# Performance work log

Measured on AMD Instinct MI355X. Metric: run time of the kernel, lower is better.

Reference implementation:

```python
import jax, jax.numpy as jnp
import numpy as np

NEG_SLOPE = 0.2
EPS = 1e-16


def sp_gat_layer(h, src, trg, w, a_src, a_trg):
    # h: [N, f_in], w: [H, f_in, f_out], a_src/a_trg: [H, f_out]
    n = h.shape[0]
    h_prime = jnp.einsum('nf,hfo->nho', h, w)            # [N, H, O]
    attn_src = jnp.einsum('nho,ho->nh', h_prime, a_src)  # [N, H]
    attn_trg = jnp.einsum('nho,ho->nh', h_prime, a_trg)  # [N, H]
    e = jax.nn.leaky_relu(attn_src[src] + attn_trg[trg], NEG_SLOPE)  # [E, H]
    e = e - e.max()  # global max-shift, as in the torch code
    exp_e = jnp.exp(e)
    denom = jax.ops.segment_sum(exp_e, trg, num_segments=n)          # [N, H]
    neigh_attn = exp_e / (denom[trg] + EPS)                          # [E, H]
    h_weighted = h_prime[src] * neigh_attn[..., None]                # [E, H, O]
    return jax.ops.segment_sum(h_weighted, trg, num_segments=n)     # [N, H, O]


def run_stack(h, src, trg, params):
    # params: list of (w, a_src, a_trg); last layer mean over heads, others elu+flatten
    n = h.shape[0]
    n_layers = len(params)
    for i, (w, a_src, a_trg) in enumerate(params):
        out = sp_gat_layer(h, src, trg, w, a_src, a_trg)  # [N, H, O]
        if i + 1 == n_layers:
            h = out.mean(axis=1)                          # [N, O]
        else:
            h = jax.nn.elu(out.reshape(n, -1))            # [N, H*O]
    return h


def setup_inputs() -> dict:
    key = jax.random.key(0)
    ks = jax.random.split(key, 24)
    N, E = 60000, 800000
    H, F0, O = 8, 128, 32
    inp = {
        'h0': jax.random.normal(ks[0], (N, F0), jnp.float32),
        'h1': jax.random.normal(ks[1], (N, F0), jnp.float32),
        'src0': jax.random.randint(ks[2], (E,), 0, N),
        'trg0': jax.random.randint(ks[3], (E,), 0, N),
        'src1': jax.random.randint(ks[4], (E,), 0, N),
        'trg1': jax.random.randint(ks[5], (E,), 0, N),
        'w00': jax.random.normal(ks[6], (H, F0, O), jnp.float32) * 0.1,
        'asrc00': jax.random.normal(ks[7], (H, O), jnp.float32) * 0.1,
        'atrg00': jax.random.normal(ks[8], (H, O), jnp.float32) * 0.1,
        'w01': jax.random.normal(ks[9], (H, H * O, O), jnp.float32) * 0.1,
        'asrc01': jax.random.normal(ks[10], (H, O), jnp.float32) * 0.1,
        'atrg01': jax.random.normal(ks[11], (H, O), jnp.float32) * 0.1,
        'w10': jax.random.normal(ks[12], (H, F0, O), jnp.float32) * 0.1,
        'asrc10': jax.random.normal(ks[13], (H, O), jnp.float32) * 0.1,
        'atrg10': jax.random.normal(ks[14], (H, O), jnp.float32) * 0.1,
        'w11': jax.random.normal(ks[15], (H, H * O, O), jnp.float32) * 0.1,
        'asrc11': jax.random.normal(ks[16], (H, O), jnp.float32) * 0.1,
        'atrg11': jax.random.normal(ks[17], (H, O), jnp.float32) * 0.1,
        'fc_w': jax.random.normal(ks[18], (2 * O, 2), jnp.float32) * 0.1,
        'fc_b': jnp.zeros((2,), jnp.float32),
    }
    return inp


N_USER = 50000


def reference(h0, h1, src0, trg0, src1, trg1,
              w00, asrc00, atrg00, w01, asrc01, atrg01,
              w10, asrc10, atrg10, w11, asrc11, atrg11,
              fc_w, fc_b):
    emb0 = run_stack(h0, src0, trg0, [(w00, asrc00, atrg00), (w01, asrc01, atrg01)])
    emb1 = run_stack(h1, src1, trg1, [(w10, asrc10, atrg10), (w11, asrc11, atrg11)])
    ret = jnp.concatenate([emb0[:N_USER], emb1[:N_USER]], axis=-1)  # [n_user, 64]
    logits = ret @ fc_w + fc_b
    return jax.nn.log_softmax(logits, axis=-1)
```

## Files before the change

### kernel.cpp

```cpp
#include <hip/hip_runtime.h>
#include <math.h>

#define H 8
#define O 32
#define C 256
#define CAP 48
#define NEG_SLOPE 0.2f
#define EPS_V 1e-16f
#define LOG2E 1.4426950408889634f

#define W_BKT 128
#define NB_PAD 512
#define BCAP 2048
#define EPB 4096

typedef float f32x4 __attribute__((ext_vector_type(4)));
typedef float f32x2 __attribute__((ext_vector_type(2)));
typedef short bf16x8 __attribute__((ext_vector_type(8)));

__device__ __forceinline__ unsigned short f2bf(float x){
  unsigned u = __float_as_uint(x);
  unsigned r = (u + 0x7fffu + ((u >> 16) & 1u)) >> 16;
  return (unsigned short)r;
}
__device__ __forceinline__ float bf2f(unsigned short u){
  return __uint_as_float((unsigned)u << 16);
}

template<int F>
__device__ __forceinline__ void cvt_a_body(const float* __restrict__ src,
                                           short* __restrict__ dst,
                                           int n_nodes, int t, int total){
  constexpr int KB = F / 8;
  if (t >= total) return;
  int kb = t % KB;
  int m  = (t / KB) & 15;
  int rt = t / (KB * 16);
  int row = rt * 16 + m;
  float v[8];
  if (row < n_nodes){
    const float4 p0 = *(const float4*)(src + (size_t)row * F + kb * 8);
    const float4 p1 = *(const float4*)(src + (size_t)row * F + kb * 8 + 4);
    v[0]=p0.x; v[1]=p0.y; v[2]=p0.z; v[3]=p0.w;
    v[4]=p1.x; v[5]=p1.y; v[6]=p1.z; v[7]=p1.w;
  } else {
    for (int j = 0; j < 8; ++j) v[j] = 0.f;
  }
  bf16x8 o;
  for (int j = 0; j < 8; ++j) o[j] = (short)f2bf(v[j]);
  *(bf16x8*)(dst + (((size_t)rt * KB + kb) * 16 + m) * 8) = o;
}

template<int F>
__device__ __forceinline__ void cvt_w_body(const float* __restrict__ w,
                                           short* __restrict__ wb, int t){
  constexpr int KB = F / 8;
  if (t >= 256 * KB) return;
  int c = t & 255, kb = t >> 8;
  int h = c >> 5, o = c & 31;
  bf16x8 out;
  for (int j = 0; j < 8; ++j){
    int f = kb * 8 + j;
    out[j] = (short)f2bf(w[((size_t)h * F + f) * O + o]);
  }
  *(bf16x8*)(wb + ((size_t)kb * 256 + c) * 8) = out;
}

__device__ void pass1_body(const int* __restrict__ trg, const int* __restrict__ src,
                           unsigned* __restrict__ gbuf, unsigned* __restrict__ gcur,
                           int E, int bx, int tid){
  __shared__ int cnt[NB_PAD];
  __shared__ int offl[NB_PAD];
  __shared__ unsigned baseg[NB_PAD];
  __shared__ int cur[NB_PAD];
  __shared__ unsigned payload[EPB];

  const int e0 = bx * EPB;
  const int ne = min(EPB, E - e0);
  for (int i = tid; i < NB_PAD; i += 256) cnt[i] = 0;
  __syncthreads();
  for (int i = tid; i < ne; i += 256){
    int t = trg[e0 + i];
    atomicAdd(&cnt[t >> 7], 1);
  }
  __syncthreads();
  for (int i = tid; i < NB_PAD; i += 256){
    int c = cnt[i];
    baseg[i] = c ? atomicAdd(&gcur[i], (unsigned)c) : 0u;
  }
  if (tid < 64){
    int v[8]; int s = 0;
#pragma unroll
    for (int j = 0; j < 8; ++j){ v[j] = cnt[tid * 8 + j]; s += v[j]; }
    int x = s;
#pragma unroll
    for (int d = 1; d < 64; d <<= 1){
      int o = __shfl_up(x, d, 64);
      if (tid >= d) x += o;
    }
    int base = x - s;
#pragma unroll
    for (int j = 0; j < 8; ++j){ offl[tid * 8 + j] = base; base += v[j]; }
  }
  __syncthreads();
  for (int i = tid; i < NB_PAD; i += 256) cur[i] = offl[i];
  __syncthreads();
  for (int i = tid; i < ne; i += 256){
    int t = trg[e0 + i];
    int s = src[e0 + i];
    int b = t >> 7;
    int p = atomicAdd(&cur[b], 1);
    payload[p] = ((unsigned)b << 23) | ((unsigned)(t & 127) << 16) | (unsigned)s;
  }
  __syncthreads();
  for (int i = tid; i < ne; i += 256){
    unsigned v = payload[i];
    unsigned b = v >> 23;
    unsigned pos = baseg[b] + (unsigned)(i - offl[b]);
    if (pos < BCAP) gbuf[(size_t)b * BCAP + pos] = v;
  }
}

__device__ void pass2_body(const unsigned* __restrict__ gbuf,
                           const unsigned* __restrict__ gcur,
                           unsigned short* __restrict__ csrc, int* __restrict__ degv,
                           int N, int bx, int tid){
  __shared__ unsigned short ell[W_BKT * CAP];
  __shared__ int dcnt[W_BKT];
  const int node0 = bx << 7;
  const int nn = min(W_BKT, N - node0);
  const unsigned pat = ((unsigned)N << 16) | (unsigned)N;
  unsigned* e32 = (unsigned*)ell;
  for (int i = tid; i < W_BKT * CAP / 2; i += 256) e32[i] = pat;
  for (int i = tid; i < W_BKT; i += 256) dcnt[i] = 0;
  __syncthreads();
  const int ne = min((int)gcur[bx], BCAP);
  for (int i = tid; i < ne; i += 256){
    unsigned v = gbuf[(size_t)bx * BCAP + i];
    int lt = (v >> 16) & 127;
    int p = atomicAdd(&dcnt[lt], 1);
    if (p < CAP) ell[lt * CAP + p] = (unsigned short)(v & 0xffffu);
  }
  __syncthreads();
  const uint4* s4 = (const uint4*)ell;
  uint4* d4 = (uint4*)(csrc + (size_t)node0 * CAP);
  const int n16 = nn * (CAP / 8);
  for (int i = tid; i < n16; i += 256) d4[i] = s4[i];
  for (int i = tid; i < nn; i += 256) degv[node0 + i] = dcnt[i];
}

template<int F>
__device__ __forceinline__ void gemm_body(
    const short* __restrict__ hb, const short* __restrict__ wb,
    const float* __restrict__ a_src, const float* __restrict__ a_trg,
    unsigned char* __restrict__ hp, float* __restrict__ as_, float* __restrict__ at_,
    int n_nodes, int bx, int tidx){
  constexpr int KB = F / 8;
  const int w = tidx >> 6, l = tidx & 63;
  const int q = l >> 4, m15 = l & 15;
  const int row0 = bx * 32;
  const size_t rt0 = row0 >> 4;
  const int ct0 = w * 4;
  float wsv[4], wtv[4];
#pragma unroll
  for (int ct = 0; ct < 4; ++ct){
    int col = (ct0 + ct) * 16 + m15;
    wsv[ct] = a_src[col];
    wtv[ct] = a_trg[col];
  }
  f32x4 acc[2][4] = {};
  for (int kk = 0; kk < F / 32; ++kk){
    const int kb0 = kk * 4 + q;
    bf16x8 a0 = *(const bf16x8*)(hb + ((rt0 * KB + kb0) * 16 + m15) * 8);
    bf16x8 a1 = *(const bf16x8*)(hb + (((rt0 + 1) * KB + kb0) * 16 + m15) * 8);
    const short* wp = wb + ((size_t)kb0 * 256 + ct0 * 16 + m15) * 8;
#pragma unroll
    for (int ct = 0; ct < 4; ++ct){
      bf16x8 b = *(const bf16x8*)(wp + ct * 128);
      acc[0][ct] = __builtin_amdgcn_mfma_f32_16x16x32_bf16(a0, b, acc[0][ct], 0, 0, 0);
      acc[1][ct] = __builtin_amdgcn_mfma_f32_16x16x32_bf16(a1, b, acc[1][ct], 0, 0, 0);
    }
  }
  float att[2][4][4] = {};
#pragma unroll
  for (int rt2 = 0; rt2 < 2; ++rt2){
    int nb = row0 + rt2 * 16 + q * 4;
#pragma unroll
    for (int ct = 0; ct < 4; ++ct){
      int col = (ct0 + ct) * 16 + m15;
      int hi = ct >> 1;
      int p01 = __builtin_amdgcn_cvt_pk_fp8_f32(acc[rt2][ct][0], acc[rt2][ct][1], 0, false);
      int p23 = __builtin_amdgcn_cvt_pk_fp8_f32(acc[rt2][ct][2], acc[rt2][ct][3], 0, false);
      unsigned char qb[4] = {(unsigned char)(p01 & 0xff),
                             (unsigned char)((p01 >> 8) & 0xff),
                             (unsigned char)(p23 & 0xff),
                             (unsigned char)((p23 >> 8) & 0xff)};
#pragma unroll
      for (int r = 0; r < 4; ++r){
        int n = nb + r;
        if (n < n_nodes) hp[(size_t)n * C + col] = qb[r];
        float vr = acc[rt2][ct][r];
        att[rt2][r][hi]     = fmaf(vr, wsv[ct], att[rt2][r][hi]);
        att[rt2][r][2 + hi] = fmaf(vr, wtv[ct], att[rt2][r][2 + hi]);
      }
    }
  }
#pragma unroll
  for (int rt2 = 0; rt2 < 2; ++rt2)
#pragma unroll
    for (int r = 0; r < 4; ++r)
#pragma unroll
      for (int k = 0; k < 4; ++k){
        float v = att[rt2][r][k];
        v += __shfl_xor(v, 1, 64);
        v += __shfl_xor(v, 2, 64);
        v += __shfl_xor(v, 4, 64);
        v += __shfl_xor(v, 8, 64);
        att[rt2][r][k] = v;
      }
  if (m15 == 0){
    int h0i = 2 * w;
#pragma unroll
    for (int rt2 = 0; rt2 < 2; ++rt2){
      int nb = row0 + rt2 * 16 + q * 4;
#pragma unroll
      for (int r = 0; r < 4; ++r){
        int n = nb + r;
        if (n < n_nodes){
          as_[n * H + h0i]     = att[rt2][r][0] * LOG2E;
          as_[n * H + h0i + 1] = att[rt2][r][1] * LOG2E;
          at_[n * H + h0i]     = att[rt2][r][2] * LOG2E;
          at_[n * H + h0i + 1] = att[rt2][r][3] * LOG2E;
        }
      }
    }
  }
}

__global__ void prep_kernel(
    const float* __restrict__ h0, const float* __restrict__ h1,
    const float* __restrict__ w000, const float* __restrict__ w100,
    const float* __restrict__ w001, const float* __restrict__ w101,
    const int* __restrict__ t0, const int* __restrict__ t1,
    const int* __restrict__ s0, const int* __restrict__ s1,
    short* __restrict__ hb, short* __restrict__ wb0, short* __restrict__ wb1,
    unsigned* __restrict__ gbuf, unsigned* __restrict__ gcur,
    float* __restrict__ as_,
    int N, int E, int tot_a, int cvtaB, int p1B,
    size_t hbStride, size_t wbStride, size_t asStride){
  int y = blockIdx.y;
  int bx = blockIdx.x;
  int tid = threadIdx.x;
  if (bx < cvtaB){
    cvt_a_body<128>(y ? h1 : h0, hb + (size_t)y * hbStride, N, bx * 256 + tid, tot_a);
    return;
  }
  bx -= cvtaB;
  if (bx < 16){
    cvt_w_body<128>(y ? w100 : w000, wb0 + (size_t)y * wbStride, bx * 256 + tid);
    return;
  }
  bx -= 16;
  if (bx < 32){
    cvt_w_body<256>(y ? w101 : w001, wb1 + (size_t)y * wbStride, bx * 256 + tid);
    return;
  }
  bx -= 32;
  if (bx < p1B){
    pass1_body(y ? t1 : t0, y ? s1 : s0,
               gbuf + (size_t)y * NB_PAD * BCAP, gcur + (size_t)y * NB_PAD,
               E, bx, tid);
    return;
  }
  if (tid < H) as_[y * asStride + (size_t)N * H + tid] = -1e30f;
}

__global__ __launch_bounds__(256) void binfill_gemm0_kernel(
    const unsigned* __restrict__ gbuf, const unsigned* __restrict__ gcur,
    unsigned short* __restrict__ csrc, int* __restrict__ cursor, int N, int P2B,
    const short* __restrict__ hb, const short* __restrict__ wb0,
    const float* __restrict__ aps0, const float* __restrict__ apt0,
    const float* __restrict__ aps1, const float* __restrict__ apt1,
    unsigned char* __restrict__ hp, float* __restrict__ as_, float* __restrict__ at_,
    size_t hbStride, size_t wbStride, size_t hpStride, size_t asStride){
  int y = blockIdx.y;
  int bx = blockIdx.x;
  if (bx < P2B){
    pass2_body(gbuf + (size_t)y * NB_PAD * BCAP, gcur + (size_t)y * NB_PAD,
               csrc + (size_t)y * N * CAP, cursor + (size_t)y * N, N, bx, threadIdx.x);
    return;
  }
  bx -= P2B;
  gemm_body<128>(hb + (size_t)y * hbStride, wb0 + (size_t)y * wbStride,
                 y ? aps1 : aps0, y ? apt1 : apt0,
                 hp + (size_t)y * hpStride, as_ + (size_t)y * asStride,
                 at_ + (size_t)y * asStride, N, bx, threadIdx.x);
}

__global__ __launch_bounds__(256) void gemm1_kernel(
    const short* __restrict__ hb, const short* __restrict__ wb1,
    const float* __restrict__ aps0, const float* __restrict__ apt0,
    const float* __restrict__ aps1, const float* __restrict__ apt1,
    unsigned char* __restrict__ hp, float* __restrict__ as_, float* __restrict__ at_,
    int N, size_t hbStride, size_t wbStride, size_t hpStride, size_t asStride){
  int y = blockIdx.y;
  gemm_body<256>(hb + (size_t)y * hbStride, wb1 + (size_t)y * wbStride,
                 y ? aps1 : aps0, y ? apt1 : apt0,
                 hp + (size_t)y * hpStride, as_ + (size_t)y * asStride,
                 at_ + (size_t)y * asStride, N, blockIdx.x, threadIdx.x);
}

template<int MODE>
__global__ __launch_bounds__(256) void gather_kernel(
    const unsigned char* __restrict__ hp,
    const float* __restrict__ as_, const float* __restrict__ at_,
    const unsigned short* __restrict__ csrc, const int* __restrict__ degv,
    float* __restrict__ ef0, float* __restrict__ ef1,
    short* __restrict__ outb, int n_nodes, int N,
    size_t hpStride, size_t asStride, size_t hbStride){
  int y = blockIdx.y;
  hp += (size_t)y * hpStride;
  as_ += (size_t)y * asStride;
  at_ += (size_t)y * asStride;
  csrc += (size_t)y * N * CAP;
  degv += (size_t)y * N;
  int wpair = (blockIdx.x * 256 + threadIdx.x) >> 6;
  int lane = threadIdx.x & 63;
  int half = lane >> 5;
  int l = lane & 31;
  int node = wpair * 2 + half;
  if (node >= n_nodes) return;
  int head = l >> 2;
  float ath = at_[node * H + head];
  int deg = degv[node];
  deg = (deg > CAP) ? CAP : deg;
  int degR = (deg + 3) & ~3;
  const unsigned short* row = csrc + (size_t)node * CAP;
  f32x2 acc[4] = {};
  float dsum = 0.f;
  ushort4 s4 = *(const ushort4*)(row);
  for (int jb = 0; jb < degR; jb += 4){
    ushort4 s4n = *(const ushort4*)(row + jb + 4);
    int ss[4] = {s4.x, s4.y, s4.z, s4.w};
    float xa[4];
#pragma unroll
    for (int i = 0; i < 4; ++i) xa[i] = as_[ss[i] * H + head];
    uint2 vv[4];
#pragma unroll
    for (int i = 0; i < 4; ++i)
      vv[i] = *(const uint2*)(hp + (size_t)ss[i] * C + l * 8);
#pragma unroll
    for (int i = 0; i < 4; ++i){
      float x = xa[i] + ath;
      x = fmaxf(x, NEG_SLOPE * x);
      float e = __builtin_amdgcn_exp2f(x);
      dsum += e;
      f32x2 ee = {e, e};
      f32x2 u0 = __builtin_amdgcn_cvt_pk_f32_fp8(vv[i].x, false);
      f32x2 u1 = __builtin_amdgcn_cvt_pk_f32_fp8(vv[i].x, true);
      f32x2 u2 = __builtin_amdgcn_cvt_pk_f32_fp8(vv[i].y, false);
      f32x2 u3 = __builtin_amdgcn_cvt_pk_f32_fp8(vv[i].y, true);
      acc[0] += u0 * ee;
      acc[1] += u1 * ee;
      acc[2] += u2 * ee;
      acc[3] += u3 * ee;
    }
    s4 = s4n;
  }
  float inv = __builtin_amdgcn_rcpf(dsum + EPS_V);
#pragma unroll
  for (int k = 0; k < 4; ++k){ acc[k].x *= inv; acc[k].y *= inv; }
  if (MODE == 0){
    bf16x8 o;
#pragma unroll
    for (int k = 0; k < 4; ++k){
      float rx = (acc[k].x > 0.f) ? acc[k].x : (__expf(acc[k].x) - 1.f);
      float ry = (acc[k].y > 0.f) ? acc[k].y : (__expf(acc[k].y) - 1.f);
      o[2*k]   = (short)f2bf(rx);
      o[2*k+1] = (short)f2bf(ry);
    }
    short* ob = outb + (size_t)y * hbStride;
    *(bf16x8*)(ob + (((size_t)(node >> 4) * 32 + l) * 16 + (node & 15)) * 8) = o;
  } else {
#pragma unroll
    for (int mask = 4; mask <= 16; mask <<= 1){
#pragma unroll
      for (int k = 0; k < 4; ++k){
        acc[k].x += __shfl_xor(acc[k].x, mask, 64);
        acc[k].y += __shfl_xor(acc[k].y, mask, 64);
      }
    }
    if (l < 4){
      float* outf = y ? ef1 : ef0;
      float4 r0 = {acc[0].x*0.125f, acc[0].y*0.125f, acc[1].x*0.125f, acc[1].y*0.125f};
      float4 r1 = {acc[2].x*0.125f, acc[2].y*0.125f, acc[3].x*0.125f, acc[3].y*0.125f};
      *(float4*)(outf + (size_t)node * O + l * 8)     = r0;
      *(float4*)(outf + (size_t)node * O + l * 8 + 4) = r1;
    }
  }
}

__global__ void final_kernel(const float* __restrict__ e0, const float* __restrict__ e1,
                             const float* __restrict__ fw, const float* __restrict__ fb,
                             float* __restrict__ out, int n_user){
  int n = blockIdx.x * 256 + threadIdx.x;
  if (n >= n_user) return;
  float l0 = fb[0], l1 = fb[1];
  const float* p0 = e0 + (size_t)n * O;
  const float* p1 = e1 + (size_t)n * O;
#pragma unroll
  for (int o = 0; o < O; ++o){
    float v = p0[o];
    l0 = fmaf(v, fw[o * 2 + 0], l0);
    l1 = fmaf(v, fw[o * 2 + 1], l1);
  }
#pragma unroll
  for (int o = 0; o < O; ++o){
    float v = p1[o];
    l0 = fmaf(v, fw[(O + o) * 2 + 0], l0);
    l1 = fmaf(v, fw[(O + o) * 2 + 1], l1);
  }
  float m = fmaxf(l0, l1);
  float lse = m + logf(expf(l0 - m) + expf(l1 - m));
  out[n * 2 + 0] = l0 - lse;
  out[n * 2 + 1] = l1 - lse;
}

extern "C" void kernel_launch(void* const* d_in, const int* in_sizes, int n_in,
                              void* d_out, int out_size, void* d_ws, size_t ws_size,
                              hipStream_t stream){
  const float* h0 = (const float*)d_in[0];
  const float* h1 = (const float*)d_in[1];
  const int* src0 = (const int*)d_in[2];
  const int* trg0 = (const int*)d_in[3];
  const int* src1 = (const int*)d_in[4];
  const int* trg1 = (const int*)d_in[5];
  const float* W [2][2] = {{(const float*)d_in[6],  (const float*)d_in[9]},
                           {(const float*)d_in[12], (const float*)d_in[15]}};
  const float* AS[2][2] = {{(const float*)d_in[7],  (const float*)d_in[10]},
                           {(const float*)d_in[13], (const float*)d_in[16]}};
  const float* AT[2][2] = {{(const float*)d_in[8],  (const float*)d_in[11]},
                           {(const float*)d_in[14], (const float*)d_in[17]}};
  const float* fc_w = (const float*)d_in[18];
  const float* fc_b = (const float*)d_in[19];
  float* out = (float*)d_out;

  const int N = in_sizes[0] / 128;
  const int E = in_sizes[2];
  const int n_user = out_size / 2;

  const int RTt = ((N + 31) / 32) * 2;

  const size_t HPS = (size_t)(N + 16) * C;
  const size_t HBS = (size_t)RTt * 32 * 16 * 8;
  const size_t WBS = (size_t)32 * 256 * 8;
  const size_t NHP = (size_t)(N + 1) * H;

  float* ws = (float*)d_ws;
  float* attn_s = ws;  ws += 2 * NHP;
  float* attn_t = ws;  ws += 2 * NHP;
  float* emb[2];
  emb[0] = ws;         ws += (size_t)n_user * O;
  emb[1] = ws;         ws += (size_t)n_user * O;
  unsigned char* hp = (unsigned char*)ws;  ws += 2 * HPS / 4;
  short* hb  = (short*)ws;  ws += 2 * HBS / 2;
  short* wb0 = (short*)ws;  ws += 2 * WBS / 2;
  short* wb1 = (short*)ws;  ws += 2 * WBS / 2;
  unsigned short* csrc = (unsigned short*)ws;  ws += (size_t)2 * N * CAP / 2;
  int* cursor = (int*)ws;  ws += (size_t)2 * N;
  unsigned* gbuf = (unsigned*)ws;  ws += (size_t)2 * NB_PAD * BCAP;
  unsigned* gcur = (unsigned*)ws;  ws += 2 * NB_PAD;

  const int gemm_grid = (N + 31) / 32;
  const int tot_a = RTt * 16 * 16;
  const int cvtaB = (tot_a + 255) / 256;
  const int NBk = (N + W_BKT - 1) / W_BKT;
  const int p1B = (E + EPB - 1) / EPB;

  hipMemsetAsync(gcur, 0, (size_t)2 * NB_PAD * sizeof(unsigned), stream);
  prep_kernel<<<dim3(cvtaB + 16 + 32 + p1B + 1, 2), 256, 0, stream>>>(
      h0, h1, W[0][0], W[1][0], W[0][1], W[1][1],
      trg0, trg1, src0, src1,
      hb, wb0, wb1, gbuf, gcur, attn_s,
      N, E, tot_a, cvtaB, p1B, HBS, WBS, NHP);
  binfill_gemm0_kernel<<<dim3(NBk + gemm_grid, 2), 256, 0, stream>>>(
      gbuf, gcur, csrc, cursor, N, NBk,
      hb, wb0, AS[0][0], AT[0][0], AS[1][0], AT[1][0],
      hp, attn_s, attn_t, HBS, WBS, HPS, NHP);
  gather_kernel<0><<<dim3((N * 32 + 255) / 256, 2), 256, 0, stream>>>(
      hp, attn_s, attn_t, csrc, cursor, nullptr, nullptr, hb, N, N, HPS, NHP, HBS);
  gemm1_kernel<<<dim3(gemm_grid, 2), 256, 0, stream>>>(
      hb, wb1, AS[0][1], AT[0][1], AS[1][1], AT[1][1],
      hp, attn_s, attn_t, N, HBS, WBS, HPS, NHP);
  gather_kernel<1><<<dim3((n_user * 32 + 255) / 256, 2), 256, 0, stream>>>(
      hp, attn_s, attn_t, csrc, cursor, emb[0], emb[1], nullptr, n_user, N,
      HPS, NHP, HBS);
  final_kernel<<<(n_user + 255) / 256, 256, 0, stream>>>(emb[0], emb[1], fc_w, fc_b,
                                                         out, n_user);
}
```

Before: 391.2 us.

## Skew the two GAT stacks so one stack's GEMM overlaps the other's gather

The two independent stacks are offset by one stage. Each new combo kernel runs one stack's projection GEMM in some blocks and the other stack's neighbour gather in the rest, so compute-bound MFMA work shares the GPU with latency-bound gather work. The bf16 activation buffer also switches from a 16-row tiled layout to plain row-major, which simplifies the gather's output store but makes the GEMM's A loads strided. The result is one more kernel launch than before.

```diff
diff --git a/kernel.cpp b/kernel.cpp
--- a/kernel.cpp
+++ b/kernel.cpp
@@ -23,9 +23,6 @@
   unsigned r = (u + 0x7fffu + ((u >> 16) & 1u)) >> 16;
   return (unsigned short)r;
 }
-__device__ __forceinline__ float bf2f(unsigned short u){
-  return __uint_as_float((unsigned)u << 16);
-}
 
 template<int F>
 __device__ __forceinline__ void cvt_a_body(const float* __restrict__ src,
@@ -33,10 +30,8 @@
                                            int n_nodes, int t, int total){
   constexpr int KB = F / 8;
   if (t >= total) return;
-  int kb = t % KB;
-  int m  = (t / KB) & 15;
-  int rt = t / (KB * 16);
-  int row = rt * 16 + m;
+  int row = t / KB;
+  int kb = t - row * KB;
   float v[8];
   if (row < n_nodes){
     const float4 p0 = *(const float4*)(src + (size_t)row * F + kb * 8);
@@ -48,7 +43,7 @@
   }
   bf16x8 o;
   for (int j = 0; j < 8; ++j) o[j] = (short)f2bf(v[j]);
-  *(bf16x8*)(dst + (((size_t)rt * KB + kb) * 16 + m) * 8) = o;
+  *(bf16x8*)(dst + (size_t)t * 8) = o;
 }
 
 template<int F>
@@ -159,7 +154,6 @@
   const int w = tidx >> 6, l = tidx & 63;
   const int q = l >> 4, m15 = l & 15;
   const int row0 = bx * 32;
-  const size_t rt0 = row0 >> 4;
   const int ct0 = w * 4;
   float wsv[4], wtv[4];
 #pragma unroll
@@ -171,8 +165,8 @@
   f32x4 acc[2][4] = {};
   for (int kk = 0; kk < F / 32; ++kk){
     const int kb0 = kk * 4 + q;
-    bf16x8 a0 = *(const bf16x8*)(hb + ((rt0 * KB + kb0) * 16 + m15) * 8);
-    bf16x8 a1 = *(const bf16x8*)(hb + (((rt0 + 1) * KB + kb0) * 16 + m15) * 8);
+    bf16x8 a0 = *(const bf16x8*)(hb + ((size_t)(row0 + m15) * KB + kb0) * 8);
+    bf16x8 a1 = *(const bf16x8*)(hb + ((size_t)(row0 + 16 + m15) * KB + kb0) * 8);
     const short* wp = wb + ((size_t)kb0 * 256 + ct0 * 16 + m15) * 8;
 #pragma unroll
     for (int ct = 0; ct < 4; ++ct){
@@ -233,6 +227,87 @@
           at_[n * H + h0i + 1] = att[rt2][r][3] * LOG2E;
         }
       }
+    }
+  }
+}
+
+template<int MODE>
+__device__ __forceinline__ void gather_body(
+    const unsigned char* __restrict__ hp,
+    const float* __restrict__ as_, const float* __restrict__ at_,
+    const unsigned short* __restrict__ csrc, const int* __restrict__ degv,
+    float* __restrict__ outf, short* __restrict__ outb,
+    int n_nodes, int N, int bx, int tid){
+  int wpair = (bx * 256 + tid) >> 6;
+  int lane = tid & 63;
+  int half = lane >> 5;
+  int l = lane & 31;
+  int node = wpair * 2 + half;
+  if (node >= n_nodes) return;
+  int head = l >> 2;
+  float ath = at_[node * H + head];
+  int deg = degv[node];
+  deg = (deg > CAP) ? CAP : deg;
+  int degR = (deg + 3) & ~3;
+  const unsigned short* row = csrc + (size_t)node * CAP;
+  f32x2 acc[4] = {};
+  float dsum = 0.f;
+  ushort4 s4 = *(const ushort4*)(row);
+  for (int jb = 0; jb < degR; jb += 4){
+    ushort4 s4n = *(const ushort4*)(row + jb + 4);
+    int ss[4] = {s4.x, s4.y, s4.z, s4.w};
+    float xa[4];
+#pragma unroll
+    for (int i = 0; i < 4; ++i) xa[i] = as_[ss[i] * H + head];
+    uint2 vv[4];
+#pragma unroll
+    for (int i = 0; i < 4; ++i)
+      vv[i] = *(const uint2*)(hp + (size_t)ss[i] * C + l * 8);
+#pragma unroll
+    for (int i = 0; i < 4; ++i){
+      float x = xa[i] + ath;
+      x = fmaxf(x, NEG_SLOPE * x);
+      float e = __builtin_amdgcn_exp2f(x);
+      dsum += e;
+      f32x2 ee = {e, e};
+      f32x2 u0 = __builtin_amdgcn_cvt_pk_f32_fp8(vv[i].x, false);
+      f32x2 u1 = __builtin_amdgcn_cvt_pk_f32_fp8(vv[i].x, true);
+      f32x2 u2 = __builtin_amdgcn_cvt_pk_f32_fp8(vv[i].y, false);
+      f32x2 u3 = __builtin_amdgcn_cvt_pk_f32_fp8(vv[i].y, true);
+      acc[0] += u0 * ee;
+      acc[1] += u1 * ee;
+      acc[2] += u2 * ee;
+      acc[3] += u3 * ee;
+    }
+    s4 = s4n;
+  }
+  float inv = __builtin_amdgcn_rcpf(dsum + EPS_V);
+#pragma unroll
+  for (int k = 0; k < 4; ++k){ acc[k].x *= inv; acc[k].y *= inv; }
+  if (MODE == 0){
+    bf16x8 o;
+#pragma unroll
+    for (int k = 0; k < 4; ++k){
+      float rx = (acc[k].x > 0.f) ? acc[k].x : (__expf(acc[k].x) - 1.f);
+      float ry = (acc[k].y > 0.f) ? acc[k].y : (__expf(acc[k].y) - 1.f);
+      o[2*k]   = (short)f2bf(rx);
+      o[2*k+1] = (short)f2bf(ry);
+    }
+    *(bf16x8*)(outb + ((size_t)node * 32 + l) * 8) = o;
+  } else {
+#pragma unroll
+    for (int mask = 4; mask <= 16; mask <<= 1){
+#pragma unroll
+      for (int k = 0; k < 4; ++k){
+        acc[k].x += __shfl_xor(acc[k].x, mask, 64);
+        acc[k].y += __shfl_xor(acc[k].y, mask, 64);
+      }
+    }
+    if (l < 4){
+      float4 r0 = {acc[0].x*0.125f, acc[0].y*0.125f, acc[1].x*0.125f, acc[1].y*0.125f};
+      float4 r1 = {acc[2].x*0.125f, acc[2].y*0.125f, acc[3].x*0.125f, acc[3].y*0.125f};
+      *(float4*)(outf + (size_t)node * O + l * 8)     = r0;
+      *(float4*)(outf + (size_t)node * O + l * 8 + 4) = r1;
     }
   }
 }
@@ -275,128 +350,41 @@
   if (tid < H) as_[y * asStride + (size_t)N * H + tid] = -1e30f;
 }
 
-__global__ __launch_bounds__(256) void binfill_gemm0_kernel(
+__global__ __launch_bounds__(256) void pass2_gemm0_kernel(
     const unsigned* __restrict__ gbuf, const unsigned* __restrict__ gcur,
-    unsigned short* __restrict__ csrc, int* __restrict__ cursor, int N, int P2B,
-    const short* __restrict__ hb, const short* __restrict__ wb0,
-    const float* __restrict__ aps0, const float* __restrict__ apt0,
-    const float* __restrict__ aps1, const float* __restrict__ apt1,
-    unsigned char* __restrict__ hp, float* __restrict__ as_, float* __restrict__ at_,
-    size_t hbStride, size_t wbStride, size_t hpStride, size_t asStride){
-  int y = blockIdx.y;
+    unsigned short* __restrict__ csrc, int* __restrict__ cursor,
+    int N, int NBk,
+    const short* __restrict__ hb0, const short* __restrict__ wb00,
+    const float* __restrict__ as00, const float* __restrict__ at00,
+    unsigned char* __restrict__ hp0, float* __restrict__ aso0,
+    float* __restrict__ ato0){
   int bx = blockIdx.x;
-  if (bx < P2B){
+  if (bx < 2 * NBk){
+    int y = bx / NBk, bb = bx - y * NBk;
     pass2_body(gbuf + (size_t)y * NB_PAD * BCAP, gcur + (size_t)y * NB_PAD,
-               csrc + (size_t)y * N * CAP, cursor + (size_t)y * N, N, bx, threadIdx.x);
+               csrc + (size_t)y * N * CAP, cursor + (size_t)y * N, N, bb, threadIdx.x);
     return;
   }
-  bx -= P2B;
-  gemm_body<128>(hb + (size_t)y * hbStride, wb0 + (size_t)y * wbStride,
-                 y ? aps1 : aps0, y ? apt1 : apt0,
-                 hp + (size_t)y * hpStride, as_ + (size_t)y * asStride,
-                 at_ + (size_t)y * asStride, N, bx, threadIdx.x);
-}
-
-__global__ __launch_bounds__(256) void gemm1_kernel(
-    const short* __restrict__ hb, const short* __restrict__ wb1,
-    const float* __restrict__ aps0, const float* __restrict__ apt0,
-    const float* __restrict__ aps1, const float* __restrict__ apt1,
-    unsigned char* __restrict__ hp, float* __restrict__ as_, float* __restrict__ at_,
-    int N, size_t hbStride, size_t wbStride, size_t hpStride, size_t asStride){
-  int y = blockIdx.y;
-  gemm_body<256>(hb + (size_t)y * hbStride, wb1 + (size_t)y * wbStride,
-                 y ? aps1 : aps0, y ? apt1 : apt0,
-                 hp + (size_t)y * hpStride, as_ + (size_t)y * asStride,
-                 at_ + (size_t)y * asStride, N, blockIdx.x, threadIdx.x);
-}
-
-template<int MODE>
-__global__ __launch_bounds__(256) void gather_kernel(
-    const unsigned char* __restrict__ hp,
-    const float* __restrict__ as_, const float* __restrict__ at_,
-    const unsigned short* __restrict__ csrc, const int* __restrict__ degv,
-    float* __restrict__ ef0, float* __restrict__ ef1,
-    short* __restrict__ outb, int n_nodes, int N,
-    size_t hpStride, size_t asStride, size_t hbStride){
-  int y = blockIdx.y;
-  hp += (size_t)y * hpStride;
-  as_ += (size_t)y * asStride;
-  at_ += (size_t)y * asStride;
-  csrc += (size_t)y * N * CAP;
-  degv += (size_t)y * N;
-  int wpair = (blockIdx.x * 256 + threadIdx.x) >> 6;
-  int lane = threadIdx.x & 63;
-  int half = lane >> 5;
-  int l = lane & 31;
-  int node = wpair * 2 + half;
-  if (node >= n_nodes) return;
-  int head = l >> 2;
-  float ath = at_[node * H + head];
-  int deg = degv[node];
-  deg = (deg > CAP) ? CAP : deg;
-  int degR = (deg + 3) & ~3;
-  const unsigned short* row = csrc + (size_t)node * CAP;
-  f32x2 acc[4] = {};
-  float dsum = 0.f;
-  ushort4 s4 = *(const ushort4*)(row);
-  for (int jb = 0; jb < degR; jb += 4){
-    ushort4 s4n = *(const ushort4*)(row + jb + 4);
-    int ss[4] = {s4.x, s4.y, s4.z, s4.w};
-    float xa[4];
-#pragma unroll
-    for (int i = 0; i < 4; ++i) xa[i] = as_[ss[i] * H + head];
-    uint2 vv[4];
-#pragma unroll
-    for (int i = 0; i < 4; ++i)
-      vv[i] = *(const uint2*)(hp + (size_t)ss[i] * C + l * 8);
-#pragma unroll
-    for (int i = 0; i < 4; ++i){
-      float x = xa[i] + ath;
-      x = fmaxf(x, NEG_SLOPE * x);
-      float e = __builtin_amdgcn_exp2f(x);
-      dsum += e;
-      f32x2 ee = {e, e};
-      f32x2 u0 = __builtin_amdgcn_cvt_pk_f32_fp8(vv[i].x, false);
-      f32x2 u1 = __builtin_amdgcn_cvt_pk_f32_fp8(vv[i].x, true);
-      f32x2 u2 = __builtin_amdgcn_cvt_pk_f32_fp8(vv[i].y, false);
-      f32x2 u3 = __builtin_amdgcn_cvt_pk_f32_fp8(vv[i].y, true);
-      acc[0] += u0 * ee;
-      acc[1] += u1 * ee;
-      acc[2] += u2 * ee;
-      acc[3] += u3 * ee;
-    }
-    s4 = s4n;
-  }
-  float inv = __builtin_amdgcn_rcpf(dsum + EPS_V);
-#pragma unroll
-  for (int k = 0; k < 4; ++k){ acc[k].x *= inv; acc[k].y *= inv; }
-  if (MODE == 0){
-    bf16x8 o;
-#pragma unroll
-    for (int k = 0; k < 4; ++k){
-      float rx = (acc[k].x > 0.f) ? acc[k].x : (__expf(acc[k].x) - 1.f);
-      float ry = (acc[k].y > 0.f) ? acc[k].y : (__expf(acc[k].y) - 1.f);
-      o[2*k]   = (short)f2bf(rx);
-      o[2*k+1] = (short)f2bf(ry);
-    }
-    short* ob = outb + (size_t)y * hbStride;
-    *(bf16x8*)(ob + (((size_t)(node >> 4) * 32 + l) * 16 + (node & 15)) * 8) = o;
+  gemm_body<128>(hb0, wb00, as00, at00, hp0, aso0, ato0, N, bx - 2 * NBk, threadIdx.x);
+}
+
+template<int F, int MODE>
+__global__ __launch_bounds__(256) void combo_kernel(
+    int GB, int N, int n_nodes,
+    const short* __restrict__ g_hb, const short* __restrict__ g_wb,
+    const float* __restrict__ g_as, const float* __restrict__ g_at,
+    unsigned char* __restrict__ g_hp, float* __restrict__ g_aso,
+    float* __restrict__ g_ato,
+    const unsigned char* __restrict__ s_hp,
+    const float* __restrict__ s_as, const float* __restrict__ s_at,
+    const unsigned short* __restrict__ s_csrc, const int* __restrict__ s_deg,
+    float* __restrict__ s_outf, short* __restrict__ s_outb){
+  if ((int)blockIdx.x < GB){
+    gemm_body<F>(g_hb, g_wb, g_as, g_at, g_hp, g_aso, g_ato, N,
+                 blockIdx.x, threadIdx.x);
   } else {
-#pragma unroll
-    for (int mask = 4; mask <= 16; mask <<= 1){
-#pragma unroll
-      for (int k = 0; k < 4; ++k){
-        acc[k].x += __shfl_xor(acc[k].x, mask, 64);
-        acc[k].y += __shfl_xor(acc[k].y, mask, 64);
-      }
-    }
-    if (l < 4){
-      float* outf = y ? ef1 : ef0;
-      float4 r0 = {acc[0].x*0.125f, acc[0].y*0.125f, acc[1].x*0.125f, acc[1].y*0.125f};
-      float4 r1 = {acc[2].x*0.125f, acc[2].y*0.125f, acc[3].x*0.125f, acc[3].y*0.125f};
-      *(float4*)(outf + (size_t)node * O + l * 8)     = r0;
-      *(float4*)(outf + (size_t)node * O + l * 8 + 4) = r1;
-    }
+    gather_body<MODE>(s_hp, s_as, s_at, s_csrc, s_deg, s_outf, s_outb,
+                      n_nodes, N, blockIdx.x - GB, threadIdx.x);
   }
 }
 
@@ -476,6 +464,15 @@
   const int cvtaB = (tot_a + 255) / 256;
   const int NBk = (N + W_BKT - 1) / W_BKT;
   const int p1B = (E + EPB - 1) / EPB;
+  const int gBN = (N * 32 + 255) / 256;
+  const int gBU = (n_user * 32 + 255) / 256;
+
+  unsigned char* hp1 = hp + HPS;
+  short* hb1 = hb + HBS;
+  float* as0 = attn_s, *as1 = attn_s + NHP;
+  float* at0 = attn_t, *at1 = attn_t + NHP;
+  unsigned short* csrc1 = csrc + (size_t)N * CAP;
+  int* deg0 = cursor, *deg1 = cursor + N;
 
   hipMemsetAsync(gcur, 0, (size_t)2 * NB_PAD * sizeof(unsigned), stream);
   prep_kernel<<<dim3(cvtaB + 16 + 32 + p1B + 1, 2), 256, 0, stream>>>(
@@ -483,18 +480,25 @@
       trg0, trg1, src0, src1,
       hb, wb0, wb1, gbuf, gcur, attn_s,
       N, E, tot_a, cvtaB, p1B, HBS, WBS, NHP);
-  binfill_gemm0_kernel<<<dim3(NBk + gemm_grid, 2), 256, 0, stream>>>(
+  pass2_gemm0_kernel<<<2 * NBk + gemm_grid, 256, 0, stream>>>(
       gbuf, gcur, csrc, cursor, N, NBk,
-      hb, wb0, AS[0][0], AT[0][0], AS[1][0], AT[1][0],
-      hp, attn_s, attn_t, HBS, WBS, HPS, NHP);
-  gather_kernel<0><<<dim3((N * 32 + 255) / 256, 2), 256, 0, stream>>>(
-      hp, attn_s, attn_t, csrc, cursor, nullptr, nullptr, hb, N, N, HPS, NHP, HBS);
-  gemm1_kernel<<<dim3(gemm_grid, 2), 256, 0, stream>>>(
-      hb, wb1, AS[0][1], AT[0][1], AS[1][1], AT[1][1],
-      hp, attn_s, attn_t, N, HBS, WBS, HPS, NHP);
-  gather_kernel<1><<<dim3((n_user * 32 + 255) / 256, 2), 256, 0, stream>>>(
-      hp, attn_s, attn_t, csrc, cursor, emb[0], emb[1], nullptr, n_user, N,
-      HPS, NHP, HBS);
+      hb, wb0, AS[0][0], AT[0][0], hp, as0, at0);
+  combo_kernel<128, 0><<<gemm_grid + gBN, 256, 0, stream>>>(
+      gemm_grid, N, N,
+      hb1, wb0 + WBS, AS[1][0], AT[1][0], hp1, as1, at1,
+      hp, as0, at0, csrc, deg0, nullptr, hb);
+  combo_kernel<256, 0><<<gemm_grid + gBN, 256, 0, stream>>>(
+      gemm_grid, N, N,
+      hb, wb1, AS[0][1], AT[0][1], hp, as0, at0,
+      hp1, as1, at1, csrc1, deg1, nullptr, hb1);
+  combo_kernel<256, 1><<<gemm_grid + gBU, 256, 0, stream>>>(
+      gemm_grid, N, n_user,
+      hb1, wb1 + WBS, AS[1][1], AT[1][1], hp1, as1, at1,
+      hp, as0, at0, csrc, deg0, emb[0], nullptr);
+  combo_kernel<256, 1><<<gBU, 256, 0, stream>>>(
+      0, N, n_user,
+      hb1, wb1 + WBS, AS[1][1], AT[1][1], hp1, as1, at1,
+      hp1, as1, at1, csrc1, deg1, emb[1], nullptr);
   final_kernel<<<(n_user + 255) / 256, 256, 0, stream>>>(emb[0], emb[1], fc_w, fc_b,
                                                          out, n_user);
 }
```

Result: slower. 478.1 us (+22.2%).

## Fuse final gather with FC/log-softmax and switch bf16 activations to row-major layout

Applied to the files above, without the earlier changes.

The second-layer gather and the final linear plus log-softmax are merged into one kernel. Each wavefront handles one user node, with its two halves covering the two graphs, and it reduces the logits by shuffles instead of writing and re-reading embedding buffers. The bf16 activation buffer moves from a tiled MFMA layout to plain row-major, with nontemporal loads in the GEMM. The GEMM's attention reduction is restructured to lower register pressure, and launch bounds now request 8 blocks per unit. This removes one kernel launch and the emb round trip through memory. In exchange, the A-operand loads become more strided and the final gather runs with 64 threads per node.

```diff
diff --git a/kernel.cpp b/kernel.cpp
--- a/kernel.cpp
+++ b/kernel.cpp
@@ -17,14 +17,12 @@
 typedef float f32x4 __attribute__((ext_vector_type(4)));
 typedef float f32x2 __attribute__((ext_vector_type(2)));
 typedef short bf16x8 __attribute__((ext_vector_type(8)));
+typedef unsigned short u16x4 __attribute__((ext_vector_type(4)));
 
 __device__ __forceinline__ unsigned short f2bf(float x){
   unsigned u = __float_as_uint(x);
   unsigned r = (u + 0x7fffu + ((u >> 16) & 1u)) >> 16;
   return (unsigned short)r;
-}
-__device__ __forceinline__ float bf2f(unsigned short u){
-  return __uint_as_float((unsigned)u << 16);
 }
 
 template<int F>
@@ -33,10 +31,8 @@
                                            int n_nodes, int t, int total){
   constexpr int KB = F / 8;
   if (t >= total) return;
-  int kb = t % KB;
-  int m  = (t / KB) & 15;
-  int rt = t / (KB * 16);
-  int row = rt * 16 + m;
+  int row = t / KB;
+  int kb = t - row * KB;
   float v[8];
   if (row < n_nodes){
     const float4 p0 = *(const float4*)(src + (size_t)row * F + kb * 8);
@@ -48,7 +44,7 @@
   }
   bf16x8 o;
   for (int j = 0; j < 8; ++j) o[j] = (short)f2bf(v[j]);
-  *(bf16x8*)(dst + (((size_t)rt * KB + kb) * 16 + m) * 8) = o;
+  *(bf16x8*)(dst + (size_t)t * 8) = o;
 }
 
 template<int F>
@@ -159,7 +155,6 @@
   const int w = tidx >> 6, l = tidx & 63;
   const int q = l >> 4, m15 = l & 15;
   const int row0 = bx * 32;
-  const size_t rt0 = row0 >> 4;
   const int ct0 = w * 4;
   float wsv[4], wtv[4];
 #pragma unroll
@@ -171,8 +166,10 @@
   f32x4 acc[2][4] = {};
   for (int kk = 0; kk < F / 32; ++kk){
     const int kb0 = kk * 4 + q;
-    bf16x8 a0 = *(const bf16x8*)(hb + ((rt0 * KB + kb0) * 16 + m15) * 8);
-    bf16x8 a1 = *(const bf16x8*)(hb + (((rt0 + 1) * KB + kb0) * 16 + m15) * 8);
+    bf16x8 a0 = __builtin_nontemporal_load(
+        (const bf16x8*)(hb + ((size_t)(row0 + m15) * KB + kb0) * 8));
+    bf16x8 a1 = __builtin_nontemporal_load(
+        (const bf16x8*)(hb + ((size_t)(row0 + 16 + m15) * KB + kb0) * 8));
     const short* wp = wb + ((size_t)kb0 * 256 + ct0 * 16 + m15) * 8;
 #pragma unroll
     for (int ct = 0; ct < 4; ++ct){
@@ -181,10 +178,10 @@
       acc[1][ct] = __builtin_amdgcn_mfma_f32_16x16x32_bf16(a1, b, acc[1][ct], 0, 0, 0);
     }
   }
-  float att[2][4][4] = {};
 #pragma unroll
   for (int rt2 = 0; rt2 < 2; ++rt2){
     int nb = row0 + rt2 * 16 + q * 4;
+    float att[4][4] = {};
 #pragma unroll
     for (int ct = 0; ct < 4; ++ct){
       int col = (ct0 + ct) * 16 + m15;
@@ -200,41 +197,74 @@
         int n = nb + r;
         if (n < n_nodes) hp[(size_t)n * C + col] = qb[r];
         float vr = acc[rt2][ct][r];
-        att[rt2][r][hi]     = fmaf(vr, wsv[ct], att[rt2][r][hi]);
-        att[rt2][r][2 + hi] = fmaf(vr, wtv[ct], att[rt2][r][2 + hi]);
+        att[r][hi]     = fmaf(vr, wsv[ct], att[r][hi]);
+        att[r][2 + hi] = fmaf(vr, wtv[ct], att[r][2 + hi]);
       }
     }
-  }
-#pragma unroll
-  for (int rt2 = 0; rt2 < 2; ++rt2)
 #pragma unroll
     for (int r = 0; r < 4; ++r)
 #pragma unroll
       for (int k = 0; k < 4; ++k){
-        float v = att[rt2][r][k];
+        float v = att[r][k];
         v += __shfl_xor(v, 1, 64);
         v += __shfl_xor(v, 2, 64);
         v += __shfl_xor(v, 4, 64);
         v += __shfl_xor(v, 8, 64);
-        att[rt2][r][k] = v;
+        att[r][k] = v;
       }
-  if (m15 == 0){
-    int h0i = 2 * w;
-#pragma unroll
-    for (int rt2 = 0; rt2 < 2; ++rt2){
-      int nb = row0 + rt2 * 16 + q * 4;
+    if (m15 == 0){
+      int h0i = 2 * w;
 #pragma unroll
       for (int r = 0; r < 4; ++r){
         int n = nb + r;
         if (n < n_nodes){
-          as_[n * H + h0i]     = att[rt2][r][0] * LOG2E;
-          as_[n * H + h0i + 1] = att[rt2][r][1] * LOG2E;
-          at_[n * H + h0i]     = att[rt2][r][2] * LOG2E;
-          at_[n * H + h0i + 1] = att[rt2][r][3] * LOG2E;
+          as_[n * H + h0i]     = att[r][0] * LOG2E;
+          as_[n * H + h0i + 1] = att[r][1] * LOG2E;
+          at_[n * H + h0i]     = att[r][2] * LOG2E;
+          at_[n * H + h0i + 1] = att[r][3] * LOG2E;
         }
       }
     }
   }
+}
+
+__device__ __forceinline__ float gather_accum(
+    const unsigned char* __restrict__ hp,
+    const float* __restrict__ as_, float ath,
+    const unsigned short* __restrict__ row, int deg, int l, int head,
+    f32x2 (&acc)[4]){
+  int degR = (deg + 3) & ~3;
+  float dsum = 0.f;
+  u16x4 s4 = __builtin_nontemporal_load((const u16x4*)row);
+  for (int jb = 0; jb < degR; jb += 4){
+    u16x4 s4n = __builtin_nontemporal_load((const u16x4*)(row + jb + 4));
+    int ss[4] = {s4[0], s4[1], s4[2], s4[3]};
+    float xa[4];
+#pragma unroll
+    for (int i = 0; i < 4; ++i) xa[i] = as_[ss[i] * H + head];
+    uint2 vv[4];
+#pragma unroll
+    for (int i = 0; i < 4; ++i)
+      vv[i] = *(const uint2*)(hp + (size_t)ss[i] * C + l * 8);
+#pragma unroll
+    for (int i = 0; i < 4; ++i){
+      float x = xa[i] + ath;
+      x = fmaxf(x, NEG_SLOPE * x);
+      float e = __builtin_amdgcn_exp2f(x);
+      dsum += e;
+      f32x2 ee = {e, e};
+      f32x2 u0 = __builtin_amdgcn_cvt_pk_f32_fp8(vv[i].x, false);
+      f32x2 u1 = __builtin_amdgcn_cvt_pk_f32_fp8(vv[i].x, true);
+      f32x2 u2 = __builtin_amdgcn_cvt_pk_f32_fp8(vv[i].y, false);
+      f32x2 u3 = __builtin_amdgcn_cvt_pk_f32_fp8(vv[i].y, true);
+      acc[0] += u0 * ee;
+      acc[1] += u1 * ee;
+      acc[2] += u2 * ee;
+      acc[3] += u3 * ee;
+    }
+    s4 = s4n;
+  }
+  return dsum;
 }
 
 __global__ void prep_kernel(
@@ -275,9 +305,9 @@
   if (tid < H) as_[y * asStride + (size_t)N * H + tid] = -1e30f;
 }
 
-__global__ __launch_bounds__(256) void binfill_gemm0_kernel(
+__global__ __launch_bounds__(256, 8) void binfill_gemm0_kernel(
     const unsigned* __restrict__ gbuf, const unsigned* __restrict__ gcur,
-    unsigned short* __restrict__ csrc, int* __restrict__ cursor, int N, int P2B,
+    unsigned short* __restrict__ csrc, int* __restrict__ cursor, int N, int NBk,
     const short* __restrict__ hb, const short* __restrict__ wb0,
     const float* __restrict__ aps0, const float* __restrict__ apt0,
     const float* __restrict__ aps1, const float* __restrict__ apt1,
@@ -285,19 +315,56 @@
     size_t hbStride, size_t wbStride, size_t hpStride, size_t asStride){
   int y = blockIdx.y;
   int bx = blockIdx.x;
-  if (bx < P2B){
+  if (bx < NBk){
     pass2_body(gbuf + (size_t)y * NB_PAD * BCAP, gcur + (size_t)y * NB_PAD,
                csrc + (size_t)y * N * CAP, cursor + (size_t)y * N, N, bx, threadIdx.x);
     return;
   }
-  bx -= P2B;
   gemm_body<128>(hb + (size_t)y * hbStride, wb0 + (size_t)y * wbStride,
                  y ? aps1 : aps0, y ? apt1 : apt0,
                  hp + (size_t)y * hpStride, as_ + (size_t)y * asStride,
-                 at_ + (size_t)y * asStride, N, bx, threadIdx.x);
-}
-
-__global__ __launch_bounds__(256) void gemm1_kernel(
+                 at_ + (size_t)y * asStride, N, bx - NBk, threadIdx.x);
+}
+
+__global__ __launch_bounds__(256) void gather0_kernel(
+    const unsigned char* __restrict__ hp,
+    const float* __restrict__ as_, const float* __restrict__ at_,
+    const unsigned short* __restrict__ csrc, const int* __restrict__ degv,
+    short* __restrict__ outb, int n_nodes, int N,
+    size_t hpStride, size_t asStride, size_t hbStride){
+  int y = blockIdx.y;
+  hp += (size_t)y * hpStride;
+  as_ += (size_t)y * asStride;
+  at_ += (size_t)y * asStride;
+  csrc += (size_t)y * N * CAP;
+  degv += (size_t)y * N;
+  outb += (size_t)y * hbStride;
+  int wpair = (blockIdx.x * 256 + threadIdx.x) >> 6;
+  int lane = threadIdx.x & 63;
+  int half = lane >> 5;
+  int l = lane & 31;
+  int node = wpair * 2 + half;
+  if (node >= n_nodes) return;
+  int head = l >> 2;
+  float ath = at_[node * H + head];
+  int deg = degv[node];
+  deg = (deg > CAP) ? CAP : deg;
+  f32x2 acc[4] = {};
+  float dsum = gather_accum(hp, as_, ath, csrc + (size_t)node * CAP, deg, l, head, acc);
+  float inv = __builtin_amdgcn_rcpf(dsum + EPS_V);
+  bf16x8 o;
+#pragma unroll
+  for (int k = 0; k < 4; ++k){
+    float ax = acc[k].x * inv, ay = acc[k].y * inv;
+    float rx = (ax > 0.f) ? ax : (__expf(ax) - 1.f);
+    float ry = (ay > 0.f) ? ay : (__expf(ay) - 1.f);
+    o[2*k]   = (short)f2bf(rx);
+    o[2*k+1] = (short)f2bf(ry);
+  }
+  *(bf16x8*)(outb + ((size_t)node * 32 + l) * 8) = o;
+}
+
+__global__ __launch_bounds__(256, 8) void gemm1_kernel(
     const short* __restrict__ hb, const short* __restrict__ wb1,
     const float* __restrict__ aps0, const float* __restrict__ apt0,
     const float* __restrict__ aps1, const float* __restrict__ apt1,
@@ -310,120 +377,62 @@
                  at_ + (size_t)y * asStride, N, blockIdx.x, threadIdx.x);
 }
 
-template<int MODE>
-__global__ __launch_bounds__(256) void gather_kernel(
-    const unsigned char* __restrict__ hp,
-    const float* __restrict__ as_, const float* __restrict__ at_,
-    const unsigned short* __restrict__ csrc, const int* __restrict__ degv,
-    float* __restrict__ ef0, float* __restrict__ ef1,
-    short* __restrict__ outb, int n_nodes, int N,
-    size_t hpStride, size_t asStride, size_t hbStride){
-  int y = blockIdx.y;
-  hp += (size_t)y * hpStride;
-  as_ += (size_t)y * asStride;
-  at_ += (size_t)y * asStride;
-  csrc += (size_t)y * N * CAP;
-  degv += (size_t)y * N;
-  int wpair = (blockIdx.x * 256 + threadIdx.x) >> 6;
+__global__ __launch_bounds__(256, 8) void gather_fc_kernel(
+    const unsigned char* __restrict__ hp, size_t hpStride,
+    const float* __restrict__ as_, const float* __restrict__ at_, size_t asStride,
+    const unsigned short* __restrict__ csrc, const int* __restrict__ degv, int N,
+    const float* __restrict__ fw, const float* __restrict__ fb,
+    float* __restrict__ out, int n_user){
+  int node = (blockIdx.x * 256 + threadIdx.x) >> 6;
+  if (node >= n_user) return;
   int lane = threadIdx.x & 63;
   int half = lane >> 5;
   int l = lane & 31;
-  int node = wpair * 2 + half;
-  if (node >= n_nodes) return;
   int head = l >> 2;
-  float ath = at_[node * H + head];
-  int deg = degv[node];
+  const unsigned char* hps = hp + (size_t)half * hpStride;
+  const float* ass = as_ + (size_t)half * asStride;
+  const float* ats = at_ + (size_t)half * asStride;
+  const unsigned short* row = csrc + (size_t)half * N * CAP + (size_t)node * CAP;
+  int deg = degv[(size_t)half * N + node];
   deg = (deg > CAP) ? CAP : deg;
-  int degR = (deg + 3) & ~3;
-  const unsigned short* row = csrc + (size_t)node * CAP;
+  float ath = ats[node * H + head];
   f32x2 acc[4] = {};
-  float dsum = 0.f;
-  ushort4 s4 = *(const ushort4*)(row);
-  for (int jb = 0; jb < degR; jb += 4){
-    ushort4 s4n = *(const ushort4*)(row + jb + 4);
-    int ss[4] = {s4.x, s4.y, s4.z, s4.w};
-    float xa[4];
-#pragma unroll
-    for (int i = 0; i < 4; ++i) xa[i] = as_[ss[i] * H + head];
-    uint2 vv[4];
-#pragma unroll
-    for (int i = 0; i < 4; ++i)
-      vv[i] = *(const uint2*)(hp + (size_t)ss[i] * C + l * 8);
-#pragma unroll
-    for (int i = 0; i < 4; ++i){
-      float x = xa[i] + ath;
-      x = fmaxf(x, NEG_SLOPE * x);
-      float e = __builtin_amdgcn_exp2f(x);
-      dsum += e;
-      f32x2 ee = {e, e};
-      f32x2 u0 = __builtin_amdgcn_cvt_pk_f32_fp8(vv[i].x, false);
-      f32x2 u1 = __builtin_amdgcn_cvt_pk_f32_fp8(vv[i].x, true);
-      f32x2 u2 = __builtin_amdgcn_cvt_pk_f32_fp8(vv[i].y, false);
-      f32x2 u3 = __builtin_amdgcn_cvt_pk_f32_fp8(vv[i].y, true);
-      acc[0] += u0 * ee;
-      acc[1] += u1 * ee;
-      acc[2] += u2 * ee;
-      acc[3] += u3 * ee;
-    }
-    s4 = s4n;
-  }
+  float dsum = gather_accum(hps, ass, ath, row, deg, l, head, acc);
   float inv = __builtin_amdgcn_rcpf(dsum + EPS_V);
 #pragma unroll
   for (int k = 0; k < 4; ++k){ acc[k].x *= inv; acc[k].y *= inv; }
-  if (MODE == 0){
-    bf16x8 o;
+#pragma unroll
+  for (int mask = 4; mask <= 16; mask <<= 1){
 #pragma unroll
     for (int k = 0; k < 4; ++k){
-      float rx = (acc[k].x > 0.f) ? acc[k].x : (__expf(acc[k].x) - 1.f);
-      float ry = (acc[k].y > 0.f) ? acc[k].y : (__expf(acc[k].y) - 1.f);
-      o[2*k]   = (short)f2bf(rx);
-      o[2*k+1] = (short)f2bf(ry);
-    }
-    short* ob = outb + (size_t)y * hbStride;
-    *(bf16x8*)(ob + (((size_t)(node >> 4) * 32 + l) * 16 + (node & 15)) * 8) = o;
-  } else {
-#pragma unroll
-    for (int mask = 4; mask <= 16; mask <<= 1){
-#pragma unroll
-      for (int k = 0; k < 4; ++k){
-        acc[k].x += __shfl_xor(acc[k].x, mask, 64);
-        acc[k].y += __shfl_xor(acc[k].y, mask, 64);
-      }
-    }
-    if (l < 4){
-      float* outf = y ? ef1 : ef0;
-      float4 r0 = {acc[0].x*0.125f, acc[0].y*0.125f, acc[1].x*0.125f, acc[1].y*0.125f};
-      float4 r1 = {acc[2].x*0.125f, acc[2].y*0.125f, acc[3].x*0.125f, acc[3].y*0.125f};
-      *(float4*)(outf + (size_t)node * O + l * 8)     = r0;
-      *(float4*)(outf + (size_t)node * O + l * 8 + 4) = r1;
-    }
-  }
-}
-
-__global__ void final_kernel(const float* __restrict__ e0, const float* __restrict__ e1,
-                             const float* __restrict__ fw, const float* __restrict__ fb,
-                             float* __restrict__ out, int n_user){
-  int n = blockIdx.x * 256 + threadIdx.x;
-  if (n >= n_user) return;
-  float l0 = fb[0], l1 = fb[1];
-  const float* p0 = e0 + (size_t)n * O;
-  const float* p1 = e1 + (size_t)n * O;
-#pragma unroll
-  for (int o = 0; o < O; ++o){
-    float v = p0[o];
-    l0 = fmaf(v, fw[o * 2 + 0], l0);
-    l1 = fmaf(v, fw[o * 2 + 1], l1);
-  }
-#pragma unroll
-  for (int o = 0; o < O; ++o){
-    float v = p1[o];
-    l0 = fmaf(v, fw[(O + o) * 2 + 0], l0);
-    l1 = fmaf(v, fw[(O + o) * 2 + 1], l1);
-  }
-  float m = fmaxf(l0, l1);
-  float lse = m + logf(expf(l0 - m) + expf(l1 - m));
-  out[n * 2 + 0] = l0 - lse;
-  out[n * 2 + 1] = l1 - lse;
+      acc[k].x += __shfl_xor(acc[k].x, mask, 64);
+      acc[k].y += __shfl_xor(acc[k].y, mask, 64);
+    }
+  }
+  float p0 = 0.f, p1 = 0.f;
+  if (l < 4){
+    float v[8] = {acc[0].x, acc[0].y, acc[1].x, acc[1].y,
+                  acc[2].x, acc[2].y, acc[3].x, acc[3].y};
+#pragma unroll
+    for (int j = 0; j < 8; ++j){
+      float e = v[j] * 0.125f;
+      int d = half * 32 + l * 8 + j;
+      p0 = fmaf(e, fw[d * 2 + 0], p0);
+      p1 = fmaf(e, fw[d * 2 + 1], p1);
+    }
+  }
+#pragma unroll
+  for (int mask = 1; mask <= 32; mask <<= 1){
+    p0 += __shfl_xor(p0, mask, 64);
+    p1 += __shfl_xor(p1, mask, 64);
+  }
+  if (lane == 0){
+    float l0 = p0 + fb[0], l1 = p1 + fb[1];
+    float m = fmaxf(l0, l1);
+    float lse = m + logf(expf(l0 - m) + expf(l1 - m));
+    out[(size_t)node * 2 + 0] = l0 - lse;
+    out[(size_t)node * 2 + 1] = l1 - lse;
+  }
 }
 
 extern "C" void kernel_launch(void* const* d_in, const int* in_sizes, int n_in,
@@ -459,9 +468,6 @@
   float* ws = (float*)d_ws;
   float* attn_s = ws;  ws += 2 * NHP;
   float* attn_t = ws;  ws += 2 * NHP;
-  float* emb[2];
-  emb[0] = ws;         ws += (size_t)n_user * O;
-  emb[1] = ws;         ws += (size_t)n_user * O;
   unsigned char* hp = (unsigned char*)ws;  ws += 2 * HPS / 4;
   short* hb  = (short*)ws;  ws += 2 * HBS / 2;
   short* wb0 = (short*)ws;  ws += 2 * WBS / 2;
@@ -476,6 +482,8 @@
   const int cvtaB = (tot_a + 255) / 256;
   const int NBk = (N + W_BKT - 1) / W_BKT;
   const int p1B = (E + EPB - 1) / EPB;
+  const int gBN = (N * 32 + 255) / 256;
+  const int gFC = (n_user * 64 + 255) / 256;
 
   hipMemsetAsync(gcur, 0, (size_t)2 * NB_PAD * sizeof(unsigned), stream);
   prep_kernel<<<dim3(cvtaB + 16 + 32 + p1B + 1, 2), 256, 0, stream>>>(
@@ -487,14 +495,11 @@
       gbuf, gcur, csrc, cursor, N, NBk,
       hb, wb0, AS[0][0], AT[0][0], AS[1][0], AT[1][0],
       hp, attn_s, attn_t, HBS, WBS, HPS, NHP);
-  gather_kernel<0><<<dim3((N * 32 + 255) / 256, 2), 256, 0, stream>>>(
-      hp, attn_s, attn_t, csrc, cursor, nullptr, nullptr, hb, N, N, HPS, NHP, HBS);
+  gather0_kernel<<<dim3(gBN, 2), 256, 0, stream>>>(
+      hp, attn_s, attn_t, csrc, cursor, hb, N, N, HPS, NHP, HBS);
   gemm1_kernel<<<dim3(gemm_grid, 2), 256, 0, stream>>>(
       hb, wb1, AS[0][1], AT[0][1], AS[1][1], AT[1][1],
       hp, attn_s, attn_t, N, HBS, WBS, HPS, NHP);
-  gather_kernel<1><<<dim3((n_user * 32 + 255) / 256, 2), 256, 0, stream>>>(
-      hp, attn_s, attn_t, csrc, cursor, emb[0], emb[1], nullptr, n_user, N,
-      HPS, NHP, HBS);
-  final_kernel<<<(n_user + 255) / 256, 256, 0, stream>>>(emb[0], emb[1], fc_w, fc_b,
-                                                         out, n_user);
-}
+  gather_fc_kernel<<<gFC, 256, 0, stream>>>(
+      hp, HPS, attn_s, attn_t, NHP, csrc, cursor, N, fc_w, fc_b, out, n_user);
+}
```

New measurement: 514.5 us. 1.31x slower.
